# Performance work log

Measured on AMD Instinct MI355X. Metric: run time of the kernel, lower is better.

Reference implementation:

```python
import jax, jax.numpy as jnp
import numpy as np

N = 8192       # nodes
F = 256        # features
RATIO = 0.5    # fraction of nodes kept
K_KEEP = int(np.ceil(RATIO * N))  # 4096, static for jit
EDGE_PROB = 0.004  # sparse binary adjacency density


def setup_inputs() -> dict:
    key = jax.random.key(0)
    kx, ka, kp = jax.random.split(key, 3)
    X = jax.random.normal(kx, (N, F), dtype=jnp.float32)
    # binary adjacency, ~EDGE_PROB density (layer treats it as dense float)
    A = (jax.random.uniform(ka, (N, N)) < EDGE_PROB).astype(jnp.float32)
    p = jax.random.normal(kp, (F, 1), dtype=jnp.float32)  # learnable kernel
    return {"X": X, "A": A, "p": p}


def reference(X, A, p):
    # y = X p / ||p||  (scores), shape (N, 1)
    p_norm = p / jnp.sqrt(jnp.sum(p * p))
    y = X @ p_norm
    scores = y[:, 0]
    # top-K node indices; boolean_mask in the original preserves original
    # node order, so sort the indices ascending
    _, idx = jax.lax.top_k(scores, K_KEEP)
    idx = jnp.sort(idx)
    # gated features: X * tanh(y), then gather kept rows
    feats = X * jnp.tanh(y)            # (N, F)
    X_pooled = feats[idx]              # (K_KEEP, F)
    # A' = A[idx, idx]
    A_pooled = A[idx][:, idx]          # (K_KEEP, K_KEEP)
    return X_pooled, A_pooled
```

## Files before the change

kernel.cpp:

```cpp
#include <hip/hip_runtime.h>
#include <math.h>

#define N_ROWS 8192
#define F_DIM  256
#define K_KEEP 4096
#define JCH    512

__global__ void k_scores(const float* __restrict__ X, const float* __restrict__ p,
                         float* __restrict__ s_out, float* __restrict__ t_out,
                         int* __restrict__ rank_arr) {
    const int tid  = threadIdx.x;
    const int wv   = tid >> 6;
    const int lane = tid & 63;
    const int row  = blockIdx.x * 4 + wv;

    const int gid = blockIdx.x * 256 + tid;
    if (gid < N_ROWS) rank_arr[gid] = 0;

    const float4 pv = ((const float4*)p)[lane];
    const float4 xv = ((const float4*)(X + (size_t)row * F_DIM))[lane];

    double d  = (double)xv.x * pv.x + (double)xv.y * pv.y
              + (double)xv.z * pv.z + (double)xv.w * pv.w;
    double pp = (double)pv.x * pv.x + (double)pv.y * pv.y
              + (double)pv.z * pv.z + (double)pv.w * pv.w;

    #pragma unroll
    for (int off = 32; off > 0; off >>= 1) {
        d  += __shfl_down(d, off);
        pp += __shfl_down(pp, off);
    }
    if (lane == 0) {
        double y = d / sqrt(pp);
        s_out[row] = (float)y;
        t_out[row] = tanhf((float)y);
    }
}

__global__ void k_rank(const float* __restrict__ s, int* __restrict__ rank_arr) {
    const int ib = blockIdx.x >> 4;
    const int jc = blockIdx.x & 15;
    __shared__ float sk[JCH];
    const int tid = threadIdx.x;

    #pragma unroll
    for (int k = tid; k < JCH; k += 256) sk[k] = s[jc * JCH + k];
    __syncthreads();

    const int   i     = ib * 256 + tid;
    const float si    = s[i];
    const int   jbase = jc * JCH;
    int cnt = 0;
    #pragma unroll 8
    for (int j = 0; j < JCH; ++j) {
        const float v = sk[j];
        cnt += (v > si) ? 1 : 0;
        cnt += ((v == si) && ((jbase + j) < i)) ? 1 : 0;
    }
    atomicAdd(&rank_arr[i], cnt);
}

__global__ void k_compact(const int* __restrict__ rank_arr, int* __restrict__ idx) {
    const int tid  = threadIdx.x;
    const int lane = tid & 63;
    const int wv   = tid >> 6;
    const int base = tid * 32;

    int c = 0;
    #pragma unroll
    for (int k = 0; k < 32; ++k) c += (rank_arr[base + k] < K_KEEP) ? 1 : 0;

    int v = c;
    #pragma unroll
    for (int off = 1; off < 64; off <<= 1) {
        int n = __shfl_up(v, off);
        if (lane >= off) v += n;
    }
    __shared__ int wsum[4];
    if (lane == 63) wsum[wv] = v;
    __syncthreads();
    int wbase = 0;
    for (int w = 0; w < wv; ++w) wbase += wsum[w];

    int pos = wbase + v - c;
    for (int k = 0; k < 32; ++k) {
        const int i = base + k;
        if (rank_arr[i] < K_KEEP) idx[pos++] = i;
    }
}

__global__ __launch_bounds__(256) void k_pool(const float* __restrict__ X,
                                              const float* __restrict__ A,
                                              const float* __restrict__ t,
                                              const int* __restrict__ idx,
                                              float* __restrict__ out0,
                                              float* __restrict__ out1) {
    __shared__ float row[N_ROWS];
    const int tid = threadIdx.x;
    const int r   = blockIdx.x;
    const int src = idx[r];

    const float4* Arow4 = (const float4*)(A + (size_t)src * N_ROWS);
    float4 tmp[8];
    #pragma unroll
    for (int k = 0; k < 8; ++k) tmp[k] = Arow4[k * 256 + tid];
    #pragma unroll
    for (int k = 0; k < 8; ++k) ((float4*)row)[k * 256 + tid] = tmp[k];

    const float tt = t[src];
    if (tid < 64) {
        float4 v = ((const float4*)(X + (size_t)src * F_DIM))[tid];
        ((float4*)(out0 + (size_t)r * F_DIM))[tid] =
            make_float4(v.x * tt, v.y * tt, v.z * tt, v.w * tt);
    }
    __syncthreads();

    const int4* idx4 = (const int4*)idx;
    float4* o4 = (float4*)(out1 + (size_t)r * K_KEEP);
    #pragma unroll
    for (int k = 0; k < 4; ++k) {
        const int4 ci = idx4[k * 256 + tid];
        float4 o;
        o.x = row[ci.x];
        o.y = row[ci.y];
        o.z = row[ci.z];
        o.w = row[ci.w];
        o4[k * 256 + tid] = o;
    }
}

extern "C" void kernel_launch(void* const* d_in, const int* in_sizes, int n_in,
                              void* d_out, int out_size, void* d_ws, size_t ws_size,
                              hipStream_t stream) {
    const float* X = (const float*)d_in[0];
    const float* A = (const float*)d_in[1];
    const float* p = (const float*)d_in[2];

    float* ws_f   = (float*)d_ws;
    float* s_arr  = ws_f;
    float* t_arr  = ws_f + N_ROWS;
    int*   rank_a = (int*)(ws_f + 2 * N_ROWS);
    int*   idx    = (int*)(ws_f + 3 * N_ROWS);

    float* out0 = (float*)d_out;
    float* out1 = out0 + (size_t)K_KEEP * F_DIM;

    k_scores <<<N_ROWS / 4, 256, 0, stream>>>(X, p, s_arr, t_arr, rank_a);
    k_rank   <<<32 * 16,    256, 0, stream>>>(s_arr, rank_a);
    k_compact<<<1,          256, 0, stream>>>(rank_a, idx);
    k_pool   <<<K_KEEP,     256, 0, stream>>>(X, A, t_arr, idx, out0, out1);
}
```

Measured before the change: 381.4 us.

## Load A rows directly into LDS, vectorize compaction reads, use nontemporal stores

The pooling kernel now stages each selected adjacency row through `global_load_lds` straight into shared memory, skipping the register round-trip. Both outputs are written with nontemporal stores, and the gather becomes 16 scalar iterations instead of 4 float4 iterations. The single-block compaction kernel loads its rank values once as int4 vectors and reuses them for counting and scattering, instead of reading global memory twice. The risks are narrower scalar output stores and relying on the compiler to insert the wait on the direct-to-LDS loads before the barrier.

```diff
diff --git a/kernel.cpp b/kernel.cpp
--- a/kernel.cpp
+++ b/kernel.cpp
@@ -1,10 +1,18 @@
 #include <hip/hip_runtime.h>
 #include <math.h>
+#include <stdint.h>
 
 #define N_ROWS 8192
 #define F_DIM  256
 #define K_KEEP 4096
 #define JCH    512
+
+typedef float nfloat4 __attribute__((ext_vector_type(4)));
+
+#define GLOBAL_LOAD_LDS16(gaddr, laddr)                                          \
+    __builtin_amdgcn_global_load_lds(                                            \
+        (const __attribute__((address_space(1))) void*)(gaddr),                  \
+        (__attribute__((address_space(3))) void*)(laddr), 16, 0, 0)
 
 __global__ void k_scores(const float* __restrict__ X, const float* __restrict__ p,
                          float* __restrict__ s_out, float* __restrict__ t_out,
@@ -64,11 +72,15 @@
     const int tid  = threadIdx.x;
     const int lane = tid & 63;
     const int wv   = tid >> 6;
-    const int base = tid * 32;
+
+    int4 ra[8];
+    #pragma unroll
+    for (int k = 0; k < 8; ++k) ra[k] = ((const int4*)rank_arr)[tid * 8 + k];
+    const int* r32 = (const int*)ra;
 
     int c = 0;
     #pragma unroll
-    for (int k = 0; k < 32; ++k) c += (rank_arr[base + k] < K_KEEP) ? 1 : 0;
+    for (int k = 0; k < 32; ++k) c += (r32[k] < K_KEEP) ? 1 : 0;
 
     int v = c;
     #pragma unroll
@@ -83,9 +95,10 @@
     for (int w = 0; w < wv; ++w) wbase += wsum[w];
 
     int pos = wbase + v - c;
+    const int base = tid * 32;
+    #pragma unroll
     for (int k = 0; k < 32; ++k) {
-        const int i = base + k;
-        if (rank_arr[i] < K_KEEP) idx[pos++] = i;
+        if (r32[k] < K_KEEP) idx[pos++] = base + k;
     }
 }
 
@@ -100,32 +113,27 @@
     const int r   = blockIdx.x;
     const int src = idx[r];
 
-    const float4* Arow4 = (const float4*)(A + (size_t)src * N_ROWS);
-    float4 tmp[8];
+    const float* Arow = A + (size_t)src * N_ROWS;
     #pragma unroll
-    for (int k = 0; k < 8; ++k) tmp[k] = Arow4[k * 256 + tid];
-    #pragma unroll
-    for (int k = 0; k < 8; ++k) ((float4*)row)[k * 256 + tid] = tmp[k];
+    for (int k = 0; k < 8; ++k) {
+        const int e = k * 1024 + tid * 4;
+        GLOBAL_LOAD_LDS16(Arow + e, &row[e]);
+    }
 
     const float tt = t[src];
     if (tid < 64) {
         float4 v = ((const float4*)(X + (size_t)src * F_DIM))[tid];
-        ((float4*)(out0 + (size_t)r * F_DIM))[tid] =
-            make_float4(v.x * tt, v.y * tt, v.z * tt, v.w * tt);
+        nfloat4 o = {v.x * tt, v.y * tt, v.z * tt, v.w * tt};
+        __builtin_nontemporal_store(o, (nfloat4*)(out0 + (size_t)r * F_DIM) + tid);
     }
     __syncthreads();
 
-    const int4* idx4 = (const int4*)idx;
-    float4* o4 = (float4*)(out1 + (size_t)r * K_KEEP);
+    float* orow = out1 + (size_t)r * K_KEEP;
     #pragma unroll
-    for (int k = 0; k < 4; ++k) {
-        const int4 ci = idx4[k * 256 + tid];
-        float4 o;
-        o.x = row[ci.x];
-        o.y = row[ci.y];
-        o.z = row[ci.z];
-        o.w = row[ci.w];
-        o4[k * 256 + tid] = o;
+    for (int k = 0; k < 16; ++k) {
+        const int c  = k * 256 + tid;
+        const int ci = idx[c];
+        __builtin_nontemporal_store(row[ci], orow + c);
     }
 }
 
```

Result: no change. 378.5 us (-0.8%).
